# Kernel optimization log

Hardware: AMD Instinct MI355X
Metric: run time of the kernel (lower is better)

The kernel has to match this reference:

```python
import jax, jax.numpy as jnp
import numpy as np

D_MODEL = 768
N_HEADS = 24
D_HEAD = 64
D_STATE = 64
CHUNK = 64
D_INNER = N_HEADS * D_HEAD  # 1536
N_LAYER = 24
B_SZ = 2
SEQ = 8192
RMS_EPS = 1.1920929e-07  # torch.finfo(float32).eps (nn.RMSNorm default eps)


def setup_inputs() -> dict:
    key = jax.random.key(0)
    ks = jax.random.split(key, 8)
    proj = N_HEADS * (1 + 2 * D_STATE)
    return {
        "hidden_states": jax.random.normal(ks[0], (B_SZ, SEQ, D_MODEL), jnp.float32),
        "norm_w": jnp.ones((D_MODEL,), jnp.float32),
        "in_proj_w": jax.random.normal(ks[1], (2 * D_INNER, D_MODEL), jnp.float32) * 0.02,
        "in_proj_b": jnp.zeros((2 * D_INNER,), jnp.float32),
        "conv_w": jax.random.normal(ks[2], (D_INNER, 1, 4), jnp.float32) * 0.25,
        "conv_b": jnp.zeros((D_INNER,), jnp.float32),
        "x_proj_w": jax.random.normal(ks[3], (proj, D_INNER), jnp.float32) * 0.02,
        "x_proj_b": jnp.zeros((proj,), jnp.float32),
        "A_log": jnp.full((N_HEADS,), float(np.log(0.5)), jnp.float32),
        "log2_alpha_base": jnp.full((N_HEADS,), -0.15, jnp.float32),
        "log2_beta": jnp.zeros((N_HEADS,), jnp.float32),
        "surprise_ema": jnp.ones((N_HEADS,), jnp.float32),
        "out_proj_w": jax.random.normal(ks[4], (D_MODEL, D_INNER), jnp.float32) * 0.02,
        "out_proj_b": jnp.zeros((D_MODEL,), jnp.float32),
        "res_gate": jnp.full((1,), 1.0 / float(np.sqrt(2 * N_LAYER)), jnp.float32),
    }


def _block_forward(hidden_states, norm_w, in_proj_w, in_proj_b, conv_w, conv_b,
                   x_proj_w, x_proj_b, A_log, log2_alpha_base, log2_beta,
                   surprise_ema, out_proj_w, out_proj_b, res_gate):
    residual = hidden_states
    b, L, _ = hidden_states.shape

    # RMSNorm
    x = hidden_states * jax.lax.rsqrt(
        jnp.mean(hidden_states ** 2, axis=-1, keepdims=True) + RMS_EPS) * norm_w

    # in_proj, split x/z
    xz = hidden_states_proj = x @ in_proj_w.T + in_proj_b
    x, z = jnp.split(xz, 2, axis=-1)  # [b, L, d_inner] each

    # causal depthwise conv1d (kernel 4, padding 3, then truncate to L)
    xc = jnp.transpose(x, (0, 2, 1))  # [b, C, L]
    xc = jax.lax.conv_general_dilated(
        xc, conv_w, window_strides=(1,), padding=[(3, 3)],
        dimension_numbers=("NCH", "OIH", "NCH"), feature_group_count=D_INNER)
    xc = xc[:, :, :L] + conv_b[None, :, None]
    x = jax.nn.silu(jnp.transpose(xc, (0, 2, 1)))  # [b, L, d_inner]

    # x_proj -> dt, B, C
    xp = (x @ x_proj_w.T + x_proj_b).reshape(b, L, N_HEADS, 1 + 2 * D_STATE)
    dt = xp[..., 0]
    B_ssm = xp[..., 1:1 + D_STATE]
    C_ssm = xp[..., 1 + D_STATE:]
    B_ssm = B_ssm / jnp.maximum(jnp.linalg.norm(B_ssm, axis=-1, keepdims=True), 1e-12)
    C_ssm = C_ssm / jnp.maximum(jnp.linalg.norm(C_ssm, axis=-1, keepdims=True), 1e-12)

    A = jnp.clip(A_log, -2.3, -0.01)[None, None, :]  # [1,1,H]
    dt_scale = jnp.clip(jax.nn.softplus(jnp.clip(dt, -10.0, 10.0)), 0.01, 10.0)
    A = jnp.clip(A * dt_scale, -20.0, -0.001)  # [b, L, H]

    X = x.reshape(b, L, N_HEADS, D_HEAD)

    # ---- chunked surprise-gated SSD (L divisible by CHUNK) ----
    n = L // CHUNK
    X_t = X.reshape(b, n, CHUNK, N_HEADS, D_HEAD).transpose(0, 3, 1, 2, 4)      # b h n c d
    A_t = A.reshape(b, n, CHUNK, N_HEADS).transpose(0, 3, 1, 2)                 # b h n c
    B_t = B_ssm.reshape(b, n, CHUNK, N_HEADS, D_STATE).transpose(0, 3, 1, 2, 4) # b h n c s
    C_t = C_ssm.reshape(b, n, CHUNK, N_HEADS, D_STATE).transpose(0, 3, 1, 2, 4) # b h n c s

    BX = jnp.einsum("bhncs,bhncd->bhnsd", B_t, X_t)
    chunk_surprise = jnp.mean(BX ** 2, axis=(-1, -2))  # [b, h, n]

    # surprise gate (training=True: EMA updated first, no_grad)
    mean_s = jax.lax.stop_gradient(jnp.mean(chunk_surprise, axis=(0, 2)))
    ema = 0.99 * surprise_ema + 0.01 * mean_s
    normalized = chunk_surprise / (ema[None, :, None] + 1e-6)
    alpha_base = 1.0 - 2.0 ** jnp.clip(log2_alpha_base, -3.32, -0.015)  # [H]
    beta = 2.0 ** jnp.clip(log2_beta, -2.0, 2.0)                        # [H]
    boost_pos = jax.nn.relu(jnp.tanh(beta[None, :, None] * normalized))
    ab = alpha_base[None, :, None]
    alpha = jnp.clip(ab + (1.0 - ab) * boost_pos, 0.01, 0.999)          # [b, h, n]

    A_mod = A_t * (1.0 - alpha)[..., None]          # b h n c
    A_cs = jnp.cumsum(A_mod, axis=-1)               # b h n c

    # intra-chunk: L[i,j] = exp(cs_i - cs_j) for i >= j
    diff = A_cs[..., :, None] - A_cs[..., None, :]  # b h n c c
    mask = jnp.tril(jnp.ones((CHUNK, CHUNK), bool))
    Lmat = jnp.where(mask, jnp.exp(diff), 0.0)
    CB = jnp.einsum("bhnid,bhnjd->bhnij", C_t, B_t)
    Y_intra = jnp.einsum("bhnij,bhnjd->bhnid", Lmat * CB, X_t)

    # inter-chunk recurrence
    decay_chunk = jnp.exp(jnp.sum(A_mod, axis=-1))              # b h n
    decay_to_end = jnp.exp(A_cs[..., -1:] - A_cs)               # b h n c
    h_chunk_final = jnp.einsum("bhnc,bhncs,bhncd->bhnsd",
                               decay_to_end, B_t, X_t)           # b h n s d

    def step(carry, inp):
        d, hf = inp  # d: [b,h], hf: [b,h,s,d]
        new = d[..., None, None] * carry + hf
        return new, carry  # emit state BEFORE this chunk

    carry0 = jnp.zeros((b, N_HEADS, D_STATE, D_HEAD), X.dtype)
    _, h_inter = jax.lax.scan(
        step, carry0,
        (decay_chunk.transpose(2, 0, 1), h_chunk_final.transpose(2, 0, 1, 3, 4)))
    h_inter = h_inter.transpose(1, 2, 0, 3, 4)  # b h n s d

    decay_from_start = jnp.exp(A_cs)  # b h n c
    Y_inter = jnp.einsum("bhnis,bhnsp,bhni->bhnip", C_t, h_inter, decay_from_start)

    Y = (Y_intra + Y_inter).transpose(0, 2, 3, 1, 4).reshape(b, L, D_INNER)

    # gate + out proj + gated residual
    y = jnp.clip(Y, -100.0, 100.0) * jax.nn.sigmoid(z)
    out = jnp.clip(y @ out_proj_w.T + out_proj_b, -100.0, 100.0)
    return residual + out * res_gate


def reference(hidden_states, norm_w, in_proj_w, in_proj_b, conv_w, conv_b,
              x_proj_w, x_proj_b, A_log, log2_alpha_base, log2_beta,
              surprise_ema, out_proj_w, out_proj_b, res_gate):
    return _block_forward(hidden_states, norm_w, in_proj_w, in_proj_b, conv_w,
                          conv_b, x_proj_w, x_proj_b, A_log, log2_alpha_base,
                          log2_beta, surprise_ema, out_proj_w, out_proj_b, res_gate)
```

## Files before the change

### kernel.cpp

```cpp
#include <hip/hip_runtime.h>
#include <hip/hip_bf16.h>
#include <cstdint>
#include <cstddef>

#define L_SEQ   8192
#define DMODEL  768
#define NHEADS  24
#define DINNER  1536
#define NPROJ   3096
#define NPROJP  3200
#define NPROJ2  3264
#define HSTR    136
#define NTOK    16384
#define SEG_T   4096
#define NSEG    4
#define RMS_EPS 1.1920929e-07f

typedef __hip_bfloat16 bf16;
typedef __attribute__((ext_vector_type(8))) short bf8v;
typedef __attribute__((ext_vector_type(4))) float f4v;

__device__ __forceinline__ float clampf(float x, float lo, float hi) {
    return fminf(fmaxf(x, lo), hi);
}
__device__ __forceinline__ float bf2f(bf16 v) { return __bfloat162float(v); }
__device__ __forceinline__ bf16  f2bf(float v) { return __float2bfloat16(v); }
__device__ __forceinline__ short f2bs(float v) {
    bf16 b = __float2bfloat16(v);
    return *reinterpret_cast<short*>(&b);
}
__device__ __forceinline__ float bs2f(short v) {
    return __uint_as_float(((unsigned)(unsigned short)v) << 16);
}
__device__ __forceinline__ void st1(float* p, float v) { *p = v; }
__device__ __forceinline__ void st1(bf16* p, float v) { *p = f2bf(v); }
__device__ __forceinline__ void st4(bf16* p, float4 v) {
    p[0] = f2bf(v.x); p[1] = f2bf(v.y); p[2] = f2bf(v.z); p[3] = f2bf(v.w);
}

#define GLOAD16(gsrc, ldst) __builtin_amdgcn_global_load_lds( \
    (const __attribute__((address_space(1))) void*)(gsrc),    \
    (__attribute__((address_space(3))) void*)(ldst), 16, 0, 0)

__global__ __launch_bounds__(256) void k_cvt(const float* __restrict__ s,
                                             bf16* __restrict__ d, int n4) {
    int i = blockIdx.x * 256 + threadIdx.x;
    if (i < n4) {
        float4 v = *(const float4*)&s[i * 4];
        st4(&d[i * 4], v);
    }
}
__global__ __launch_bounds__(256) void k_zero(bf16* __restrict__ d, int n) {
    int i = blockIdx.x * 256 + threadIdx.x;
    if (i < n) d[i] = f2bf(0.f);
}

__global__ __launch_bounds__(256) void k_rmsnorm(const float* __restrict__ hs,
                                                 const float* __restrict__ w,
                                                 bf16* __restrict__ xn) {
    int t = blockIdx.x;
    const float* p = hs + (size_t)t * DMODEL;
    float s = 0.f;
    for (int i = threadIdx.x; i < DMODEL; i += 256) { float v = p[i]; s += v * v; }
    for (int off = 32; off; off >>= 1) s += __shfl_xor(s, off, 64);
    __shared__ float ws4[4];
    int lane = threadIdx.x & 63, wv = threadIdx.x >> 6;
    if (lane == 0) ws4[wv] = s;
    __syncthreads();
    s = ws4[0] + ws4[1] + ws4[2] + ws4[3];
    float r = 1.0f / sqrtf(s * (1.0f / DMODEL) + RMS_EPS);
    bf16* o = xn + (size_t)t * DMODEL;
    for (int i = threadIdx.x; i < DMODEL; i += 256) o[i] = f2bf(p[i] * r * w[i]);
}

template <typename TC, int EPI>
__global__ __launch_bounds__(256) void k_mgemm(const bf16* __restrict__ A,
                                               const bf16* __restrict__ B,
                                               const float* __restrict__ bias,
                                               TC* __restrict__ C,
                                               int M, int N, int K,
                                               const float* __restrict__ resid,
                                               const float* __restrict__ gatep) {
    __shared__ short As[2][128 * 32];
    __shared__ short Bs[2][128 * 32];
    int tid = threadIdx.x;
    int lane = tid & 63, w = tid >> 6;

    int gx = gridDim.x, gy = gridDim.y;
    int bid = blockIdx.y * gx + blockIdx.x;
    int xcd = bid & 7, idx = bid >> 3;
    int bys = gy >> 3;
    int gby = bys < 8 ? bys : 8;
    int sg  = idx / (gx * gby);
    int rem = idx - sg * (gx * gby);
    int bx  = rem / gby;
    int byl = rem - bx * gby;
    int by  = xcd * bys + sg * gby + byl;
    int m0 = by * 128, n0 = bx * 128;

    int wm = (w >> 1) << 6, wn = (w & 1) << 6;

    const size_t rowskip = (size_t)16 * K * 2;
    const char* Ag = (const char*)(A + (size_t)(m0 + (w << 5) + (lane >> 2)) * K) + (lane & 3) * 16;
    const char* Bg = (const char*)(B + (size_t)(n0 + (w << 5) + (lane >> 2)) * K) + (lane & 3) * 16;
    short* Al0 = &As[0][(w << 5) * 32];
    short* Bl0 = &Bs[0][(w << 5) * 32];
    short* Al1 = &As[1][(w << 5) * 32];
    short* Bl1 = &Bs[1][(w << 5) * 32];

    f4v acc[4][4];
#pragma unroll
    for (int i = 0; i < 4; ++i)
#pragma unroll
        for (int j = 0; j < 4; ++j) acc[i][j] = (f4v){0.f, 0.f, 0.f, 0.f};

    auto stage = [&](int buf, int k0) {
        size_t kb = (size_t)k0 * 2;
        short* Al = buf ? Al1 : Al0;
        short* Bl = buf ? Bl1 : Bl0;
        GLOAD16(Ag + kb,           Al);
        GLOAD16(Ag + kb + rowskip, Al + 16 * 32);
        GLOAD16(Bg + kb,           Bl);
        GLOAD16(Bg + kb + rowskip, Bl + 16 * 32);
    };

    stage(0, 0);
    int cur = 0;
    int row16 = lane & 15, kg = (lane >> 4) << 3;
    for (int k0 = 0; k0 < K; k0 += 32) {
        __syncthreads();
        if (k0 + 32 < K) stage(cur ^ 1, k0 + 32);
        const short* Ab = As[cur];
        const short* Bb = Bs[cur];
        bf8v af[4], bfv[4];
#pragma unroll
        for (int fm = 0; fm < 4; ++fm)
            af[fm] = *(const bf8v*)&Ab[(wm + (fm << 4) + row16) * 32 + kg];
#pragma unroll
        for (int fn = 0; fn < 4; ++fn)
            bfv[fn] = *(const bf8v*)&Bb[(wn + (fn << 4) + row16) * 32 + kg];
#pragma unroll
        for (int fm = 0; fm < 4; ++fm)
#pragma unroll
            for (int fn = 0; fn < 4; ++fn)
                acc[fm][fn] = __builtin_amdgcn_mfma_f32_16x16x32_bf16(
                    af[fm], bfv[fn], acc[fm][fn], 0, 0, 0);
        cur ^= 1;
    }

    float gate = (EPI == 1) ? *gatep : 0.f;
    int rbase = m0 + wm + ((lane >> 4) << 2);
#pragma unroll
    for (int fn = 0; fn < 4; ++fn) {
        int col = n0 + wn + (fn << 4) + (lane & 15);
        if (col >= N) continue;
        float bc = bias[col];
        int dst = col;
        if (EPI == 2) {
            int hh = col / 129, q = col - hh * 129;
            dst = hh * HSTR + (q == 0 ? 0 : q + 7);
        }
#pragma unroll
        for (int fm = 0; fm < 4; ++fm) {
#pragma unroll
            for (int r = 0; r < 4; ++r) {
                int row = rbase + (fm << 4) + r;
                float v = acc[fm][fn][r] + bc;
                if (EPI == 1) {
                    v = resid[(size_t)row * N + col] + clampf(v, -100.f, 100.f) * gate;
                    st1(&C[(size_t)row * N + col], v);
                } else if (EPI == 2) {
                    st1(&C[(size_t)row * NPROJ2 + dst], v);
                } else {
                    st1(&C[(size_t)row * N + col], v);
                }
            }
        }
    }
}

__global__ __launch_bounds__(256) void k_save_halo(const bf16* __restrict__ x,
                                                   bf16* __restrict__ dst) {
    int i = blockIdx.x * 256 + threadIdx.x;
    if (i < 3 * DINNER) dst[i] = x[(size_t)(SEG_T - 3) * DINNER + i];
}

__global__ __launch_bounds__(192) void k_conv8(const bf16* __restrict__ x,
                                               const float* __restrict__ cw,
                                               const float* __restrict__ cb,
                                               bf16* __restrict__ xc) {
    int c0 = threadIdx.x * 8;
    int r  = blockIdx.x;
    int l  = r & (L_SEQ - 1);
    float acc[8];
#pragma unroll
    for (int j = 0; j < 8; ++j) acc[j] = cb[c0 + j];
#pragma unroll
    for (int k = 0; k < 4; ++k) {
        int lp = l - 3 + k;
        if (lp < 0) continue;
        bf8v v = *(const bf8v*)(const void*)(x + (size_t)(r - 3 + k) * DINNER + c0);
#pragma unroll
        for (int j = 0; j < 8; ++j)
            acc[j] += cw[(c0 + j) * 4 + k] * bs2f(v[j]);
    }
    bf8v o;
#pragma unroll
    for (int j = 0; j < 8; ++j) {
        float a = acc[j];
        o[j] = f2bs(a / (1.f + expf(-a)));
    }
    *(bf8v*)(xc + (size_t)r * DINNER + c0) = o;
}

__global__ __launch_bounds__(256) void k_conv_silu(const bf16* __restrict__ x,
                                                   const bf16* __restrict__ xh,
                                                   const float* __restrict__ cw,
                                                   const float* __restrict__ cb,
                                                   bf16* __restrict__ xc,
                                                   int l0) {
    int c = blockIdx.x * 256 + threadIdx.x;
    int r = blockIdx.y;
    int l = l0 + r;
    float acc = cb[c];
#pragma unroll
    for (int k = 0; k < 4; ++k) {
        int lp = l - 3 + k;
        if (lp < 0) continue;
        float v = (lp < l0) ? bf2f(xh[(size_t)(lp - l0 + 3) * DINNER + c])
                            : bf2f(x[(size_t)(lp - l0) * DINNER + c]);
        acc += cw[c * 4 + k] * v;
    }
    float sig = 1.f / (1.f + expf(-acc));
    xc[(size_t)r * DINNER + c] = f2bf(acc * sig);
}

__global__ __launch_bounds__(256) void k_prep(const bf16* __restrict__ xp,
                                              const float* __restrict__ A_log,
                                              float* __restrict__ Aarr,
                                              float* __restrict__ invB,
                                              float* __restrict__ invC) {
    int wv = threadIdx.x >> 6, lane = threadIdx.x & 63;
    int idx = blockIdx.x * 4 + wv;
    int t = idx / 24, h = idx - t * 24;
    const bf16* base = xp + (size_t)t * NPROJ2 + h * HSTR;
    float b = bf2f(base[8 + lane]), c = bf2f(base[72 + lane]);
    float sb = b * b, sc = c * c;
    for (int off = 32; off; off >>= 1) {
        sb += __shfl_xor(sb, off, 64);
        sc += __shfl_xor(sc, off, 64);
    }
    if (lane == 0) {
        invB[idx] = 1.f / fmaxf(sqrtf(sb), 1e-12f);
        invC[idx] = 1.f / fmaxf(sqrtf(sc), 1e-12f);
        float dt = clampf(bf2f(base[0]), -10.f, 10.f);
        float dts = clampf(log1pf(expf(dt)), 0.01f, 10.f);
        float A = clampf(A_log[h], -2.3f, -0.01f) * dts;
        Aarr[idx] = clampf(A, -20.f, -0.001f);
    }
}

__global__ __launch_bounds__(256) void k_surprise_all(const bf16* __restrict__ xp,
                                                      const bf16* __restrict__ xc,
                                                      const float* __restrict__ invB,
                                                      float* __restrict__ cs) {
    int g = blockIdx.x;
    int cg = g / 24, h = g - cg * 24;
    int b = cg >> 7, nl = cg & 127;
    int t0 = cg * 64;
    size_t cs_idx = (size_t)(b * 24 + h) * 128 + nl;
    __shared__ short Ws[64 * 72];
    __shared__ short Xt[64 * 72];
    int tid = threadIdx.x;
#pragma unroll
    for (int half = 0; half < 2; ++half) {
        int tau = tid + half * 256;
        int c = tau >> 3, s0 = (tau & 7) << 3;
        int t = t0 + c;
        float ib = invB[t * 24 + h];
        bf8v Bv = *(const bf8v*)(const void*)(xp + (size_t)t * NPROJ2 + h * HSTR + 8 + s0);
        bf8v Xv = *(const bf8v*)(const void*)(xc + (size_t)t * DINNER + h * 64 + s0);
#pragma unroll
        for (int u = 0; u < 8; ++u) {
            Ws[(s0 + u) * 72 + c] = f2bs(bs2f(Bv[u]) * ib);
            Xt[(s0 + u) * 72 + c] = Xv[u];
        }
    }
    __syncthreads();
    int w = tid >> 6, lane = tid & 63;
    int r16 = lane & 15, kq = (lane >> 4) << 3;
    int strip = w << 4;
    f4v acc[4];
#pragma unroll
    for (int dt = 0; dt < 4; ++dt) acc[dt] = (f4v){0.f, 0.f, 0.f, 0.f};
#pragma unroll
    for (int ks = 0; ks < 2; ++ks) {
        bf8v af = *(const bf8v*)&Ws[(strip + r16) * 72 + ks * 32 + kq];
#pragma unroll
        for (int dt = 0; dt < 4; ++dt) {
            bf8v bf_ = *(const bf8v*)&Xt[((dt << 4) + r16) * 72 + ks * 32 + kq];
            acc[dt] = __builtin_amdgcn_mfma_f32_16x16x32_bf16(af, bf_, acc[dt], 0, 0, 0);
        }
    }
    float ss = 0.f;
#pragma unroll
    for (int dt = 0; dt < 4; ++dt)
#pragma unroll
        for (int r = 0; r < 4; ++r) ss += acc[dt][r] * acc[dt][r];
    for (int off = 32; off; off >>= 1) ss += __shfl_xor(ss, off, 64);
    __shared__ float ws4[4];
    if (lane == 0) ws4[w] = ss;
    __syncthreads();
    if (tid == 0) cs[cs_idx] = (ws4[0] + ws4[1] + ws4[2] + ws4[3]) * (1.f / 4096.f);
}

__global__ __launch_bounds__(256) void k_alpha(const float* __restrict__ cs,
                                               const float* __restrict__ ema0,
                                               const float* __restrict__ l2ab,
                                               const float* __restrict__ l2b,
                                               float* __restrict__ alpha) {
    int h = blockIdx.x, tid = threadIdx.x;
    int b = tid >> 7, n = tid & 127;
    int gi = (b * 24 + h) * 128 + n;
    float v = cs[gi];
    float s = v;
    for (int off = 32; off; off >>= 1) s += __shfl_xor(s, off, 64);
    __shared__ float ws4[4];
    int lane = tid & 63, wv = tid >> 6;
    if (lane == 0) ws4[wv] = s;
    __syncthreads();
    float total = ws4[0] + ws4[1] + ws4[2] + ws4[3];
    float ema = 0.99f * ema0[h] + 0.01f * (total * (1.f / 256.f));
    float ab = 1.f - exp2f(clampf(l2ab[h], -3.32f, -0.015f));
    float beta = exp2f(clampf(l2b[h], -2.f, 2.f));
    float nz = v / (ema + 1e-6f);
    float boost = fmaxf(tanhf(beta * nz), 0.f);
    alpha[gi] = clampf(ab + (1.f - ab) * boost, 0.01f, 0.999f);
}

__device__ __forceinline__ void chunk_body(const bf16* xp, const bf16* xc,
                                           const float* invB, const float* invC,
                                           const float* Aarr, const float* alpha,
                                           bf16* ybuf, bf16* hf, float* dchunk,
                                           int t0, int h, size_t gidx, size_t hbase) {
    float alp = alpha[gidx];
    __shared__ short Cs[64 * 72];
    __shared__ short Bs[64 * 72];
    __shared__ short Ws[64 * 72];
    __shared__ short Xt[64 * 72];
    __shared__ float Acs[64];
    __shared__ float dte[64];
    int tid = threadIdx.x;
    if (tid < 64) {
        float a = Aarr[(size_t)(t0 + tid) * 24 + h] * (1.f - alp);
        for (int off = 1; off < 64; off <<= 1) {
            float u = __shfl_up(a, off, 64);
            if (tid >= off) a += u;
        }
        Acs[tid] = a;
        float total = __shfl(a, 63, 64);
        dte[tid] = expf(total - a);
        if (tid == 0) dchunk[gidx] = expf(total);
    }
    __syncthreads();
#pragma unroll
    for (int half = 0; half < 2; ++half) {
        int tau = tid + half * 256;
        int c = tau >> 3, s0 = (tau & 7) << 3;
        int t = t0 + c;
        const bf16* bp = xp + (size_t)t * NPROJ2 + h * HSTR;
        float ib = invB[t * 24 + h], ic2 = invC[t * 24 + h];
        float dc = dte[c];
        bf8v Bv = *(const bf8v*)(const void*)(bp + 8 + s0);
        bf8v Cv = *(const bf8v*)(const void*)(bp + 72 + s0);
        bf8v Xv = *(const bf8v*)(const void*)(xc + (size_t)t * DINNER + h * 64 + s0);
        bf8v Bsc, Csc;
#pragma unroll
        for (int u = 0; u < 8; ++u) {
            float bv = bs2f(Bv[u]) * ib;
            Bsc[u] = f2bs(bv);
            Csc[u] = f2bs(bs2f(Cv[u]) * ic2);
            Ws[(s0 + u) * 72 + c] = f2bs(bv * dc);
            Xt[(s0 + u) * 72 + c] = Xv[u];
        }
        *(bf8v*)&Bs[c * 72 + s0] = Bsc;
        *(bf8v*)&Cs[c * 72 + s0] = Csc;
    }
    __syncthreads();
    int w = tid >> 6, lane = tid & 63;
    int r16 = lane & 15, kq = (lane >> 4) << 3;
    int strip = w << 4;
    f4v acb[4], ach[4];
#pragma unroll
    for (int jt = 0; jt < 4; ++jt) {
        acb[jt] = (f4v){0.f, 0.f, 0.f, 0.f};
        ach[jt] = (f4v){0.f, 0.f, 0.f, 0.f};
    }
#pragma unroll
    for (int ks = 0; ks < 2; ++ks) {
        bf8v afc = *(const bf8v*)&Cs[(strip + r16) * 72 + ks * 32 + kq];
        bf8v afw = *(const bf8v*)&Ws[(strip + r16) * 72 + ks * 32 + kq];
#pragma unroll
        for (int jt = 0; jt < 4; ++jt) {
            bf8v bb = *(const bf8v*)&Bs[((jt << 4) + r16) * 72 + ks * 32 + kq];
            acb[jt] = __builtin_amdgcn_mfma_f32_16x16x32_bf16(afc, bb, acb[jt], 0, 0, 0);
            bf8v xx = *(const bf8v*)&Xt[((jt << 4) + r16) * 72 + ks * 32 + kq];
            ach[jt] = __builtin_amdgcn_mfma_f32_16x16x32_bf16(afw, xx, ach[jt], 0, 0, 0);
        }
    }
    int rbase = strip + ((lane >> 4) << 2);
#pragma unroll
    for (int dt = 0; dt < 4; ++dt) {
        int d = (dt << 4) + r16;
#pragma unroll
        for (int r = 0; r < 4; ++r)
            hf[hbase + (size_t)(rbase + r) * 64 + d] = f2bf(ach[dt][r]);
    }
    __syncthreads();
    short* Ms = Cs;
#pragma unroll
    for (int jt = 0; jt < 4; ++jt) {
        int j = (jt << 4) + r16;
        float aj = Acs[j];
#pragma unroll
        for (int r = 0; r < 4; ++r) {
            int i = rbase + r;
            float m = (j <= i) ? expf(Acs[i] - aj) * acb[jt][r] : 0.f;
            Ms[i * 72 + j] = f2bs(m);
        }
    }
    __syncthreads();
    f4v acy[4];
#pragma unroll
    for (int dt = 0; dt < 4; ++dt) acy[dt] = (f4v){0.f, 0.f, 0.f, 0.f};
#pragma unroll
    for (int ks = 0; ks < 2; ++ks) {
        bf8v afm = *(const bf8v*)&Ms[(strip + r16) * 72 + ks * 32 + kq];
#pragma unroll
        for (int dt = 0; dt < 4; ++dt) {
            bf8v xx = *(const bf8v*)&Xt[((dt << 4) + r16) * 72 + ks * 32 + kq];
            acy[dt] = __builtin_amdgcn_mfma_f32_16x16x32_bf16(afm, xx, acy[dt], 0, 0, 0);
        }
    }
#pragma unroll
    for (int dt = 0; dt < 4; ++dt) {
        int d = (dt << 4) + r16;
#pragma unroll
        for (int r = 0; r < 4; ++r) {
            int i = rbase + r;
            ybuf[(size_t)(t0 + i) * DINNER + h * 64 + d] = f2bf(acy[dt][r]);
        }
    }
}

__global__ __launch_bounds__(256) void k_chunk(const bf16* __restrict__ xp,
                                               const bf16* __restrict__ xc,
                                               const float* __restrict__ invB,
                                               const float* __restrict__ invC,
                                               const float* __restrict__ Aarr,
                                               const float* __restrict__ alpha,
                                               bf16* __restrict__ ybuf,
                                               bf16* __restrict__ hf,
                                               float* __restrict__ dchunk,
                                               int b, int l0) {
    int g = blockIdx.x;
    int h = g >> 6, nl = g & 63;
    chunk_body(xp, xc, invB, invC, Aarr, alpha, ybuf, hf, dchunk,
               nl * 64, h,
               (size_t)(b * 24 + h) * 128 + (l0 >> 6) + nl,
               (size_t)((h << 6) + nl) * 4096);
}

__global__ __launch_bounds__(256) void k_chunk_all(const bf16* __restrict__ xp,
                                                   const bf16* __restrict__ xc,
                                                   const float* __restrict__ invB,
                                                   const float* __restrict__ invC,
                                                   const float* __restrict__ Aarr,
                                                   const float* __restrict__ alpha,
                                                   bf16* __restrict__ ybuf,
                                                   bf16* __restrict__ hf,
                                                   float* __restrict__ dchunk) {
    int g = blockIdx.x;
    int bh = g >> 7, nl = g & 127;
    int b = bh >= 24 ? 1 : 0, h = bh - b * 24;
    size_t gidx = (size_t)bh * 128 + nl;
    chunk_body(xp, xc, invB, invC, Aarr, alpha, ybuf, hf, dchunk,
               b * L_SEQ + nl * 64, h, gidx, gidx * 4096);
}

__global__ __launch_bounds__(256) void k_scan(bf16* __restrict__ hf,
                                              const float* __restrict__ dchunk,
                                              float* __restrict__ carry,
                                              int b, int l0, int nch) {
    int h = blockIdx.x >> 4;
    int e = ((blockIdx.x & 15) << 8) + threadIdx.x;
    int bh = b * 24 + h;
    float c = (l0 == 0) ? 0.f : carry[(size_t)bh * 4096 + e];
    size_t a = (size_t)h * nch * 4096 + e;
    float v = bf2f(hf[a]);
    const float* dcp = dchunk + (size_t)bh * 128 + (l0 >> 6);
    for (int nl = 0; nl < nch; ++nl) {
        float dc = dcp[nl];
        float vn = (nl + 1 < nch) ? bf2f(hf[a + 4096]) : 0.f;
        hf[a] = f2bf(c);
        c = dc * c + v;
        v = vn;
        a += 4096;
    }
    carry[(size_t)bh * 4096 + e] = c;
}

__global__ __launch_bounds__(256) void k_scan_all(bf16* __restrict__ hf,
                                                  const float* __restrict__ dchunk) {
    int bh = blockIdx.x >> 4;
    int e = ((blockIdx.x & 15) << 8) + threadIdx.x;
    float c = 0.f;
    size_t a = (size_t)bh * 128 * 4096 + e;
    float v = bf2f(hf[a]);
    const float* dcp = dchunk + (size_t)bh * 128;
    for (int nl = 0; nl < 128; ++nl) {
        float dc = dcp[nl];
        float vn = (nl + 1 < 128) ? bf2f(hf[a + 4096]) : 0.f;
        hf[a] = f2bf(c);
        c = dc * c + v;
        v = vn;
        a += 4096;
    }
}

__device__ __forceinline__ void inter_body(const bf16* xp, const float* invC,
                                           const float* Aarr, const float* alpha,
                                           const bf16* hf, const bf16* zbuf,
                                           bf16* ybuf,
                                           int t0, int h, size_t gidx, size_t hbase) {
    float alp = alpha[gidx];
    __shared__ short Cs[64 * 72];
    __shared__ short Ht[64 * 72];
    __shared__ float dfs[64];
    int tid = threadIdx.x;
    if (tid < 64) {
        float a = Aarr[(size_t)(t0 + tid) * 24 + h] * (1.f - alp);
        for (int off = 1; off < 64; off <<= 1) {
            float u = __shfl_up(a, off, 64);
            if (tid >= off) a += u;
        }
        dfs[tid] = expf(a);
    }
#pragma unroll
    for (int half = 0; half < 2; ++half) {
        int tau = tid + half * 256;
        int c = tau >> 3, s0 = (tau & 7) << 3;
        int t = t0 + c;
        float ic2 = invC[t * 24 + h];
        bf8v Cv = *(const bf8v*)(const void*)(xp + (size_t)t * NPROJ2 + h * HSTR + 72 + s0);
        bf8v Hv = *(const bf8v*)(const void*)(hf + hbase + (size_t)c * 64 + s0);
        bf8v Csc;
#pragma unroll
        for (int u = 0; u < 8; ++u) {
            Csc[u] = f2bs(bs2f(Cv[u]) * ic2);
            Ht[(s0 + u) * 72 + c] = Hv[u];
        }
        *(bf8v*)&Cs[c * 72 + s0] = Csc;
    }
    __syncthreads();
    int w = tid >> 6, lane = tid & 63;
    int r16 = lane & 15, kq = (lane >> 4) << 3;
    int strip = w << 4;
    f4v acc[4];
#pragma unroll
    for (int dt = 0; dt < 4; ++dt) acc[dt] = (f4v){0.f, 0.f, 0.f, 0.f};
#pragma unroll
    for (int ks = 0; ks < 2; ++ks) {
        bf8v af = *(const bf8v*)&Cs[(strip + r16) * 72 + ks * 32 + kq];
#pragma unroll
        for (int dt = 0; dt < 4; ++dt) {
            bf8v hfr = *(const bf8v*)&Ht[((dt << 4) + r16) * 72 + ks * 32 + kq];
            acc[dt] = __builtin_amdgcn_mfma_f32_16x16x32_bf16(af, hfr, acc[dt], 0, 0, 0);
        }
    }
    int ibase = strip + ((lane >> 4) << 2);
#pragma unroll
    for (int dt = 0; dt < 4; ++dt) {
        int d = (dt << 4) + r16;
#pragma unroll
        for (int r = 0; r < 4; ++r) {
            int i = ibase + r;
            float df = dfs[i];
            size_t yoff = (size_t)(t0 + i) * DINNER + h * 64 + d;
            float Y = clampf(bf2f(ybuf[yoff]) + df * acc[dt][r], -100.f, 100.f);
            float zz = bf2f(zbuf[yoff]);
            ybuf[yoff] = f2bf(Y / (1.f + expf(-zz)));
        }
    }
}

__global__ __launch_bounds__(256) void k_inter(const bf16* __restrict__ xp,
                                               const float* __restrict__ invC,
                                               const float* __restrict__ Aarr,
                                               const float* __restrict__ alpha,
                                               const bf16* __restrict__ hf,
                                               const bf16* __restrict__ zbuf,
                                               bf16* __restrict__ ybuf,
                                               int b, int l0) {
    int g = blockIdx.x;
    int h = g >> 6, nl = g & 63;
    inter_body(xp, invC, Aarr, alpha, hf, zbuf, ybuf,
               nl * 64, h,
               (size_t)(b * 24 + h) * 128 + (l0 >> 6) + nl,
               (size_t)((h << 6) + nl) * 4096);
}

__global__ __launch_bounds__(256) void k_inter_all(const bf16* __restrict__ xp,
                                                   const float* __restrict__ invC,
                                                   const float* __restrict__ Aarr,
                                                   const float* __restrict__ alpha,
                                                   const bf16* __restrict__ hf,
                                                   const bf16* __restrict__ zbuf,
                                                   bf16* __restrict__ ybuf) {
    int g = blockIdx.x;
    int bh = g >> 7, nl = g & 127;
    int b = bh >= 24 ? 1 : 0, h = bh - b * 24;
    size_t gidx = (size_t)bh * 128 + nl;
    inter_body(xp, invC, Aarr, alpha, hf, zbuf, ybuf,
               b * L_SEQ + nl * 64, h, gidx, gidx * 4096);
}

extern "C" void kernel_launch(void* const* d_in, const int* in_sizes, int n_in,
                              void* d_out, int out_size, void* d_ws, size_t ws_size,
                              hipStream_t stream) {
    const float* hs     = (const float*)d_in[0];
    const float* norm_w = (const float*)d_in[1];
    const float* w1     = (const float*)d_in[2];
    const float* b1     = (const float*)d_in[3];
    const float* cw     = (const float*)d_in[4];
    const float* cbias  = (const float*)d_in[5];
    const float* w2     = (const float*)d_in[6];
    const float* b2     = (const float*)d_in[7];
    const float* A_log  = (const float*)d_in[8];
    const float* l2ab   = (const float*)d_in[9];
    const float* l2b    = (const float*)d_in[10];
    const float* ema0   = (const float*)d_in[11];
    const float* w3     = (const float*)d_in[12];
    const float* b3     = (const float*)d_in[13];
    const float* rg     = (const float*)d_in[14];
    float* out = (float*)d_out;

    const bool FULL = ws_size >= (size_t)255500000;
    const size_t YROWS = FULL ? (size_t)NTOK : (size_t)SEG_T;

    char* base = (char*)d_ws;
    size_t off = 0;
    auto alloc = [&](size_t bytes) -> void* {
        void* p = base + off;
        off += (bytes + 255) & ~(size_t)255;
        return p;
    };
    bf16* w1bf  = (bf16*)alloc((size_t)2 * DINNER * DMODEL * 2);
    bf16* w2bf  = (bf16*)alloc((size_t)NPROJP * DINNER * 2);
    bf16* w3bf  = (bf16*)alloc((size_t)DMODEL * DINNER * 2);
    bf16* xn    = (bf16*)alloc((size_t)NTOK * DMODEL * 2);
    bf16* ybuf  = (bf16*)alloc(YROWS * DINNER * 2);
    bf16* hf    = (bf16*)alloc(YROWS / 64 * NHEADS * 4096 * 2);
    bf16* xhalo = (bf16*)alloc((size_t)2 * 3 * DINNER * 2);
    float* cs   = (float*)alloc((size_t)6144 * 4);
    float* alp  = (float*)alloc((size_t)6144 * 4);
    float* dch  = (float*)alloc((size_t)6144 * 4);
    float* carry= (float*)alloc((size_t)48 * 4096 * 4);
    bf16* xp    = (bf16*)alloc((size_t)NTOK * NPROJ2 * 2);
    float* Aarr = (float*)alloc((size_t)NTOK * 24 * 4);
    float* invB = (float*)alloc((size_t)NTOK * 24 * 4);
    float* invC = (float*)alloc((size_t)NTOK * 24 * 4);
    bf16* xbuf  = ybuf;
    bf16* xc_all = (bf16*)d_out;

    {
        int n1 = 2 * DINNER * DMODEL / 4, n2 = NPROJ * DINNER / 4, n3 = DMODEL * DINNER / 4;
        k_cvt<<<(n1 + 255) / 256, 256, 0, stream>>>(w1, w1bf, n1);
        k_cvt<<<(n2 + 255) / 256, 256, 0, stream>>>(w2, w2bf, n2);
        k_cvt<<<(n3 + 255) / 256, 256, 0, stream>>>(w3, w3bf, n3);
        int nz = (NPROJP - NPROJ) * DINNER;
        k_zero<<<(nz + 255) / 256, 256, 0, stream>>>(w2bf + (size_t)NPROJ * DINNER, nz);
    }

    const dim3 gPall(NPROJP / 128, NTOK / 128);

    if (FULL) {
        const dim3 gX16(DINNER / 128, NTOK / 128);
        const dim3 gO16(DMODEL / 128, NTOK / 128);
        k_rmsnorm<<<NTOK, 256, 0, stream>>>(hs, norm_w, xn);
        k_mgemm<bf16, 0><<<gX16, 256, 0, stream>>>(xn, w1bf, b1, xbuf,
                                                   NTOK, DINNER, DMODEL, nullptr, nullptr);
        k_conv8<<<NTOK, 192, 0, stream>>>(xbuf, cw, cbias, xc_all);
        k_mgemm<bf16, 2><<<gPall, 256, 0, stream>>>(xc_all, w2bf, b2, xp,
                                                    NTOK, NPROJ, DINNER, nullptr, nullptr);
        k_prep<<<NTOK * 24 / 4, 256, 0, stream>>>(xp, A_log, Aarr, invB, invC);
        k_surprise_all<<<6144, 256, 0, stream>>>(xp, xc_all, invB, cs);
        k_alpha<<<24, 256, 0, stream>>>(cs, ema0, l2ab, l2b, alp);

        k_chunk_all<<<6144, 256, 0, stream>>>(xp, xc_all, invB, invC, Aarr, alp,
                                              ybuf, hf, dch);
        k_mgemm<bf16, 0><<<gX16, 256, 0, stream>>>(xn, w1bf + (size_t)DINNER * DMODEL,
                                                   b1 + DINNER, xc_all,
                                                   NTOK, DINNER, DMODEL, nullptr, nullptr);
        k_scan_all<<<768, 256, 0, stream>>>(hf, dch);
        k_inter_all<<<6144, 256, 0, stream>>>(xp, invC, Aarr, alp, hf, xc_all, ybuf);
        k_mgemm<float, 1><<<gO16, 256, 0, stream>>>(ybuf, w3bf, b3, out,
                                                    NTOK, DMODEL, DINNER, hs, rg);
        return;
    }

    const dim3 gX(DINNER / 128, SEG_T / 128);
    const dim3 gO(DMODEL / 128, SEG_T / 128);

    k_rmsnorm<<<NTOK, 256, 0, stream>>>(hs, norm_w, xn);
    for (int s = 0; s < NSEG; ++s) {
        size_t t0 = (size_t)s * SEG_T;
        int l0 = (int)(t0 & (L_SEQ - 1));
        bf16* xc = xc_all + t0 * DINNER;
        k_mgemm<bf16, 0><<<gX, 256, 0, stream>>>(xn + t0 * DMODEL, w1bf, b1, xbuf,
                                                 SEG_T, DINNER, DMODEL, nullptr, nullptr);
        k_save_halo<<<18, 256, 0, stream>>>(xbuf, xhalo + (size_t)((s + 1) & 1) * 3 * DINNER);
        k_conv_silu<<<dim3(DINNER / 256, SEG_T), 256, 0, stream>>>(
            xbuf, xhalo + (size_t)(s & 1) * 3 * DINNER, cw, cbias, xc, l0);
    }
    k_mgemm<bf16, 2><<<gPall, 256, 0, stream>>>(xc_all, w2bf, b2, xp,
                                                NTOK, NPROJ, DINNER, nullptr, nullptr);
    k_prep<<<NTOK * 24 / 4, 256, 0, stream>>>(xp, A_log, Aarr, invB, invC);
    k_surprise_all<<<6144, 256, 0, stream>>>(xp, xc_all, invB, cs);
    k_alpha<<<24, 256, 0, stream>>>(cs, ema0, l2ab, l2b, alp);

    for (int s = 0; s < NSEG; ++s) {
        size_t t0 = (size_t)s * SEG_T;
        int l0 = (int)(t0 & (L_SEQ - 1));
        int b  = (int)(t0 >> 13);
        const float* hseg = hs + t0 * DMODEL;
        bf16* xc = xc_all + t0 * DINNER;
        bf16* zseg = xc;
        const bf16* xpS = xp + t0 * NPROJ2;
        const float* AarrS = Aarr + t0 * 24;
        const float* invBS = invB + t0 * 24;
        const float* invCS = invC + t0 * 24;
        k_chunk<<<NHEADS * 64, 256, 0, stream>>>(xpS, xc, invBS, invCS, AarrS, alp,
                                                 ybuf, hf, dch, b, l0);
        k_mgemm<bf16, 0><<<gX, 256, 0, stream>>>(xn + t0 * DMODEL,
                                                 w1bf + (size_t)DINNER * DMODEL,
                                                 b1 + DINNER, zseg,
                                                 SEG_T, DINNER, DMODEL, nullptr, nullptr);
        k_scan<<<384, 256, 0, stream>>>(hf, dch, carry, b, l0, 64);
        k_inter<<<NHEADS * 64, 256, 0, stream>>>(xpS, invCS, AarrS, alp, hf, zseg,
                                                 ybuf, b, l0);
        k_mgemm<float, 1><<<gO, 256, 0, stream>>>(ybuf, w3bf, b3, out + t0 * DMODEL,
                                                  SEG_T, DMODEL, DINNER, hseg, rg);
    }
}
```

Measured before the change: 907.4 us.

## Segment by batch, compact projection buffer, and split dt into its own array

This removes the dual FULL/segmented schedule and always processes the two batch sequences one after another, in 8192-token segments. Each segment aligns with a sequence boundary, so the halo-save kernel and the scalar conv kernel go away in favour of the vectorised conv8 kernel. The x_proj output is packed to a 3072-wide B/C layout, and dt is written by the GEMM epilogue into a separate small buffer, which cuts padding and read traffic. In exchange, RMSNorm is recomputed per segment to keep the normalised buffer small. The schedule also uses more launches than a single full-size pass.

Measured after the change: 932.0 us. 2.7% more time.

```diff
diff --git a/kernel.cpp b/kernel.cpp
--- a/kernel.cpp
+++ b/kernel.cpp
@@ -9,11 +9,9 @@
 #define DINNER  1536
 #define NPROJ   3096
 #define NPROJP  3200
-#define NPROJ2  3264
-#define HSTR    136
+#define XPS     3072
 #define NTOK    16384
-#define SEG_T   4096
-#define NSEG    4
+#define BT      8192
 #define RMS_EPS 1.1920929e-07f
 
 typedef __hip_bfloat16 bf16;
@@ -80,7 +78,8 @@
                                                TC* __restrict__ C,
                                                int M, int N, int K,
                                                const float* __restrict__ resid,
-                                               const float* __restrict__ gatep) {
+                                               const float* __restrict__ gatep,
+                                               bf16* __restrict__ dtb) {
     __shared__ short As[2][128 * 32];
     __shared__ short Bs[2][128 * 32];
     int tid = threadIdx.x;
@@ -155,10 +154,11 @@
         int col = n0 + wn + (fn << 4) + (lane & 15);
         if (col >= N) continue;
         float bc = bias[col];
-        int dst = col;
+        int hh = 0, dst = col;
         if (EPI == 2) {
-            int hh = col / 129, q = col - hh * 129;
-            dst = hh * HSTR + (q == 0 ? 0 : q + 7);
+            hh = col / 129;
+            int q = col - hh * 129;
+            dst = (q == 0) ? -1 : hh * 128 + q - 1;
         }
 #pragma unroll
         for (int fm = 0; fm < 4; ++fm) {
@@ -170,19 +170,14 @@
                     v = resid[(size_t)row * N + col] + clampf(v, -100.f, 100.f) * gate;
                     st1(&C[(size_t)row * N + col], v);
                 } else if (EPI == 2) {
-                    st1(&C[(size_t)row * NPROJ2 + dst], v);
+                    if (dst < 0) dtb[(size_t)row * 24 + hh] = f2bf(v);
+                    else st1(&C[(size_t)row * XPS + dst], v);
                 } else {
                     st1(&C[(size_t)row * N + col], v);
                 }
             }
         }
     }
-}
-
-__global__ __launch_bounds__(256) void k_save_halo(const bf16* __restrict__ x,
-                                                   bf16* __restrict__ dst) {
-    int i = blockIdx.x * 256 + threadIdx.x;
-    if (i < 3 * DINNER) dst[i] = x[(size_t)(SEG_T - 3) * DINNER + i];
 }
 
 __global__ __launch_bounds__(192) void k_conv8(const bf16* __restrict__ x,
@@ -191,15 +186,14 @@
                                                bf16* __restrict__ xc) {
     int c0 = threadIdx.x * 8;
     int r  = blockIdx.x;
-    int l  = r & (L_SEQ - 1);
     float acc[8];
 #pragma unroll
     for (int j = 0; j < 8; ++j) acc[j] = cb[c0 + j];
 #pragma unroll
     for (int k = 0; k < 4; ++k) {
-        int lp = l - 3 + k;
+        int lp = r - 3 + k;
         if (lp < 0) continue;
-        bf8v v = *(const bf8v*)(const void*)(x + (size_t)(r - 3 + k) * DINNER + c0);
+        bf8v v = *(const bf8v*)(const void*)(x + (size_t)lp * DINNER + c0);
 #pragma unroll
         for (int j = 0; j < 8; ++j)
             acc[j] += cw[(c0 + j) * 4 + k] * bs2f(v[j]);
@@ -213,29 +207,8 @@
     *(bf8v*)(xc + (size_t)r * DINNER + c0) = o;
 }
 
-__global__ __launch_bounds__(256) void k_conv_silu(const bf16* __restrict__ x,
-                                                   const bf16* __restrict__ xh,
-                                                   const float* __restrict__ cw,
-                                                   const float* __restrict__ cb,
-                                                   bf16* __restrict__ xc,
-                                                   int l0) {
-    int c = blockIdx.x * 256 + threadIdx.x;
-    int r = blockIdx.y;
-    int l = l0 + r;
-    float acc = cb[c];
-#pragma unroll
-    for (int k = 0; k < 4; ++k) {
-        int lp = l - 3 + k;
-        if (lp < 0) continue;
-        float v = (lp < l0) ? bf2f(xh[(size_t)(lp - l0 + 3) * DINNER + c])
-                            : bf2f(x[(size_t)(lp - l0) * DINNER + c]);
-        acc += cw[c * 4 + k] * v;
-    }
-    float sig = 1.f / (1.f + expf(-acc));
-    xc[(size_t)r * DINNER + c] = f2bf(acc * sig);
-}
-
 __global__ __launch_bounds__(256) void k_prep(const bf16* __restrict__ xp,
+                                              const bf16* __restrict__ dtb,
                                               const float* __restrict__ A_log,
                                               float* __restrict__ Aarr,
                                               float* __restrict__ invB,
@@ -243,8 +216,8 @@
     int wv = threadIdx.x >> 6, lane = threadIdx.x & 63;
     int idx = blockIdx.x * 4 + wv;
     int t = idx / 24, h = idx - t * 24;
-    const bf16* base = xp + (size_t)t * NPROJ2 + h * HSTR;
-    float b = bf2f(base[8 + lane]), c = bf2f(base[72 + lane]);
+    const bf16* base = xp + (size_t)t * XPS + h * 128;
+    float b = bf2f(base[lane]), c = bf2f(base[64 + lane]);
     float sb = b * b, sc = c * c;
     for (int off = 32; off; off >>= 1) {
         sb += __shfl_xor(sb, off, 64);
@@ -253,7 +226,7 @@
     if (lane == 0) {
         invB[idx] = 1.f / fmaxf(sqrtf(sb), 1e-12f);
         invC[idx] = 1.f / fmaxf(sqrtf(sc), 1e-12f);
-        float dt = clampf(bf2f(base[0]), -10.f, 10.f);
+        float dt = clampf(bf2f(dtb[idx]), -10.f, 10.f);
         float dts = clampf(log1pf(expf(dt)), 0.01f, 10.f);
         float A = clampf(A_log[h], -2.3f, -0.01f) * dts;
         Aarr[idx] = clampf(A, -20.f, -0.001f);
@@ -278,7 +251,7 @@
         int c = tau >> 3, s0 = (tau & 7) << 3;
         int t = t0 + c;
         float ib = invB[t * 24 + h];
-        bf8v Bv = *(const bf8v*)(const void*)(xp + (size_t)t * NPROJ2 + h * HSTR + 8 + s0);
+        bf8v Bv = *(const bf8v*)(const void*)(xp + (size_t)t * XPS + h * 128 + s0);
         bf8v Xv = *(const bf8v*)(const void*)(xc + (size_t)t * DINNER + h * 64 + s0);
 #pragma unroll
         for (int u = 0; u < 8; ++u) {
@@ -338,11 +311,21 @@
     alpha[gi] = clampf(ab + (1.f - ab) * boost, 0.01f, 0.999f);
 }
 
-__device__ __forceinline__ void chunk_body(const bf16* xp, const bf16* xc,
-                                           const float* invB, const float* invC,
-                                           const float* Aarr, const float* alpha,
-                                           bf16* ybuf, bf16* hf, float* dchunk,
-                                           int t0, int h, size_t gidx, size_t hbase) {
+__global__ __launch_bounds__(256) void k_chunk(const bf16* __restrict__ xp,
+                                               const bf16* __restrict__ xc,
+                                               const float* __restrict__ invB,
+                                               const float* __restrict__ invC,
+                                               const float* __restrict__ Aarr,
+                                               const float* __restrict__ alpha,
+                                               bf16* __restrict__ ybuf,
+                                               bf16* __restrict__ hf,
+                                               float* __restrict__ dchunk,
+                                               int b) {
+    int g = blockIdx.x;
+    int h = g >> 7, nl = g & 127;
+    int t0 = nl * 64;
+    size_t gidx = (size_t)(b * 24 + h) * 128 + nl;
+    size_t hbase = (size_t)g * 4096;
     float alp = alpha[gidx];
     __shared__ short Cs[64 * 72];
     __shared__ short Bs[64 * 72];
@@ -368,11 +351,11 @@
         int tau = tid + half * 256;
         int c = tau >> 3, s0 = (tau & 7) << 3;
         int t = t0 + c;
-        const bf16* bp = xp + (size_t)t * NPROJ2 + h * HSTR;
+        const bf16* bp = xp + (size_t)t * XPS + h * 128;
         float ib = invB[t * 24 + h], ic2 = invC[t * 24 + h];
         float dc = dte[c];
-        bf8v Bv = *(const bf8v*)(const void*)(bp + 8 + s0);
-        bf8v Cv = *(const bf8v*)(const void*)(bp + 72 + s0);
+        bf8v Bv = *(const bf8v*)(const void*)(bp + s0);
+        bf8v Cv = *(const bf8v*)(const void*)(bp + 64 + s0);
         bf8v Xv = *(const bf8v*)(const void*)(xc + (size_t)t * DINNER + h * 64 + s0);
         bf8v Bsc, Csc;
 #pragma unroll
@@ -453,71 +436,15 @@
     }
 }
 
-__global__ __launch_bounds__(256) void k_chunk(const bf16* __restrict__ xp,
-                                               const bf16* __restrict__ xc,
-                                               const float* __restrict__ invB,
-                                               const float* __restrict__ invC,
-                                               const float* __restrict__ Aarr,
-                                               const float* __restrict__ alpha,
-                                               bf16* __restrict__ ybuf,
-                                               bf16* __restrict__ hf,
-                                               float* __restrict__ dchunk,
-                                               int b, int l0) {
-    int g = blockIdx.x;
-    int h = g >> 6, nl = g & 63;
-    chunk_body(xp, xc, invB, invC, Aarr, alpha, ybuf, hf, dchunk,
-               nl * 64, h,
-               (size_t)(b * 24 + h) * 128 + (l0 >> 6) + nl,
-               (size_t)((h << 6) + nl) * 4096);
-}
-
-__global__ __launch_bounds__(256) void k_chunk_all(const bf16* __restrict__ xp,
-                                                   const bf16* __restrict__ xc,
-                                                   const float* __restrict__ invB,
-                                                   const float* __restrict__ invC,
-                                                   const float* __restrict__ Aarr,
-                                                   const float* __restrict__ alpha,
-                                                   bf16* __restrict__ ybuf,
-                                                   bf16* __restrict__ hf,
-                                                   float* __restrict__ dchunk) {
-    int g = blockIdx.x;
-    int bh = g >> 7, nl = g & 127;
-    int b = bh >= 24 ? 1 : 0, h = bh - b * 24;
-    size_t gidx = (size_t)bh * 128 + nl;
-    chunk_body(xp, xc, invB, invC, Aarr, alpha, ybuf, hf, dchunk,
-               b * L_SEQ + nl * 64, h, gidx, gidx * 4096);
-}
-
 __global__ __launch_bounds__(256) void k_scan(bf16* __restrict__ hf,
                                               const float* __restrict__ dchunk,
-                                              float* __restrict__ carry,
-                                              int b, int l0, int nch) {
+                                              int b) {
     int h = blockIdx.x >> 4;
     int e = ((blockIdx.x & 15) << 8) + threadIdx.x;
-    int bh = b * 24 + h;
-    float c = (l0 == 0) ? 0.f : carry[(size_t)bh * 4096 + e];
-    size_t a = (size_t)h * nch * 4096 + e;
+    float c = 0.f;
+    size_t a = (size_t)h * 128 * 4096 + e;
     float v = bf2f(hf[a]);
-    const float* dcp = dchunk + (size_t)bh * 128 + (l0 >> 6);
-    for (int nl = 0; nl < nch; ++nl) {
-        float dc = dcp[nl];
-        float vn = (nl + 1 < nch) ? bf2f(hf[a + 4096]) : 0.f;
-        hf[a] = f2bf(c);
-        c = dc * c + v;
-        v = vn;
-        a += 4096;
-    }
-    carry[(size_t)bh * 4096 + e] = c;
-}
-
-__global__ __launch_bounds__(256) void k_scan_all(bf16* __restrict__ hf,
-                                                  const float* __restrict__ dchunk) {
-    int bh = blockIdx.x >> 4;
-    int e = ((blockIdx.x & 15) << 8) + threadIdx.x;
-    float c = 0.f;
-    size_t a = (size_t)bh * 128 * 4096 + e;
-    float v = bf2f(hf[a]);
-    const float* dcp = dchunk + (size_t)bh * 128;
+    const float* dcp = dchunk + (size_t)(b * 24 + h) * 128;
     for (int nl = 0; nl < 128; ++nl) {
         float dc = dcp[nl];
         float vn = (nl + 1 < 128) ? bf2f(hf[a + 4096]) : 0.f;
@@ -528,11 +455,19 @@
     }
 }
 
-__device__ __forceinline__ void inter_body(const bf16* xp, const float* invC,
-                                           const float* Aarr, const float* alpha,
-                                           const bf16* hf, const bf16* zbuf,
-                                           bf16* ybuf,
-                                           int t0, int h, size_t gidx, size_t hbase) {
+__global__ __launch_bounds__(256) void k_inter(const bf16* __restrict__ xp,
+                                               const float* __restrict__ invC,
+                                               const float* __restrict__ Aarr,
+                                               const float* __restrict__ alpha,
+                                               const bf16* __restrict__ hf,
+                                               const bf16* __restrict__ zbuf,
+                                               bf16* __restrict__ ybuf,
+                                               int b) {
+    int g = blockIdx.x;
+    int h = g >> 7, nl = g & 127;
+    int t0 = nl * 64;
+    size_t gidx = (size_t)(b * 24 + h) * 128 + nl;
+    size_t hbase = (size_t)g * 4096;
     float alp = alpha[gidx];
     __shared__ short Cs[64 * 72];
     __shared__ short Ht[64 * 72];
@@ -552,7 +487,7 @@
         int c = tau >> 3, s0 = (tau & 7) << 3;
         int t = t0 + c;
         float ic2 = invC[t * 24 + h];
-        bf8v Cv = *(const bf8v*)(const void*)(xp + (size_t)t * NPROJ2 + h * HSTR + 72 + s0);
+        bf8v Cv = *(const bf8v*)(const void*)(xp + (size_t)t * XPS + h * 128 + 64 + s0);
         bf8v Hv = *(const bf8v*)(const void*)(hf + hbase + (size_t)c * 64 + s0);
         bf8v Csc;
 #pragma unroll
@@ -592,37 +527,6 @@
             ybuf[yoff] = f2bf(Y / (1.f + expf(-zz)));
         }
     }
-}
-
-__global__ __launch_bounds__(256) void k_inter(const bf16* __restrict__ xp,
-                                               const float* __restrict__ invC,
-                                               const float* __restrict__ Aarr,
-                                               const float* __restrict__ alpha,
-                                               const bf16* __restrict__ hf,
-                                               const bf16* __restrict__ zbuf,
-                                               bf16* __restrict__ ybuf,
-                                               int b, int l0) {
-    int g = blockIdx.x;
-    int h = g >> 6, nl = g & 63;
-    inter_body(xp, invC, Aarr, alpha, hf, zbuf, ybuf,
-               nl * 64, h,
-               (size_t)(b * 24 + h) * 128 + (l0 >> 6) + nl,
-               (size_t)((h << 6) + nl) * 4096);
-}
-
-__global__ __launch_bounds__(256) void k_inter_all(const bf16* __restrict__ xp,
-                                                   const float* __restrict__ invC,
-                                                   const float* __restrict__ Aarr,
-                                                   const float* __restrict__ alpha,
-                                                   const bf16* __restrict__ hf,
-                                                   const bf16* __restrict__ zbuf,
-                                                   bf16* __restrict__ ybuf) {
-    int g = blockIdx.x;
-    int bh = g >> 7, nl = g & 127;
-    int b = bh >= 24 ? 1 : 0, h = bh - b * 24;
-    size_t gidx = (size_t)bh * 128 + nl;
-    inter_body(xp, invC, Aarr, alpha, hf, zbuf, ybuf,
-               b * L_SEQ + nl * 64, h, gidx, gidx * 4096);
 }
 
 extern "C" void kernel_launch(void* const* d_in, const int* in_sizes, int n_in,
@@ -645,9 +549,6 @@
     const float* rg     = (const float*)d_in[14];
     float* out = (float*)d_out;
 
-    const bool FULL = ws_size >= (size_t)255500000;
-    const size_t YROWS = FULL ? (size_t)NTOK : (size_t)SEG_T;
-
     char* base = (char*)d_ws;
     size_t off = 0;
     auto alloc = [&](size_t bytes) -> void* {
@@ -658,15 +559,14 @@
     bf16* w1bf  = (bf16*)alloc((size_t)2 * DINNER * DMODEL * 2);
     bf16* w2bf  = (bf16*)alloc((size_t)NPROJP * DINNER * 2);
     bf16* w3bf  = (bf16*)alloc((size_t)DMODEL * DINNER * 2);
-    bf16* xn    = (bf16*)alloc((size_t)NTOK * DMODEL * 2);
-    bf16* ybuf  = (bf16*)alloc(YROWS * DINNER * 2);
-    bf16* hf    = (bf16*)alloc(YROWS / 64 * NHEADS * 4096 * 2);
-    bf16* xhalo = (bf16*)alloc((size_t)2 * 3 * DINNER * 2);
+    bf16* xnb   = (bf16*)alloc((size_t)BT * DMODEL * 2);
+    bf16* ybuf  = (bf16*)alloc((size_t)BT * DINNER * 2);
+    bf16* hf    = (bf16*)alloc((size_t)NHEADS * 128 * 4096 * 2);
+    bf16* dtb   = (bf16*)alloc((size_t)NTOK * 24 * 2);
     float* cs   = (float*)alloc((size_t)6144 * 4);
     float* alp  = (float*)alloc((size_t)6144 * 4);
     float* dch  = (float*)alloc((size_t)6144 * 4);
-    float* carry= (float*)alloc((size_t)48 * 4096 * 4);
-    bf16* xp    = (bf16*)alloc((size_t)NTOK * NPROJ2 * 2);
+    bf16* xp    = (bf16*)alloc((size_t)NTOK * XPS * 2);
     float* Aarr = (float*)alloc((size_t)NTOK * 24 * 4);
     float* invB = (float*)alloc((size_t)NTOK * 24 * 4);
     float* invC = (float*)alloc((size_t)NTOK * 24 * 4);
@@ -682,74 +582,41 @@
         k_zero<<<(nz + 255) / 256, 256, 0, stream>>>(w2bf + (size_t)NPROJ * DINNER, nz);
     }
 
+    const dim3 gXb(DINNER / 128, BT / 128);
+    const dim3 gOb(DMODEL / 128, BT / 128);
     const dim3 gPall(NPROJP / 128, NTOK / 128);
 
-    if (FULL) {
-        const dim3 gX16(DINNER / 128, NTOK / 128);
-        const dim3 gO16(DMODEL / 128, NTOK / 128);
-        k_rmsnorm<<<NTOK, 256, 0, stream>>>(hs, norm_w, xn);
-        k_mgemm<bf16, 0><<<gX16, 256, 0, stream>>>(xn, w1bf, b1, xbuf,
-                                                   NTOK, DINNER, DMODEL, nullptr, nullptr);
-        k_conv8<<<NTOK, 192, 0, stream>>>(xbuf, cw, cbias, xc_all);
-        k_mgemm<bf16, 2><<<gPall, 256, 0, stream>>>(xc_all, w2bf, b2, xp,
-                                                    NTOK, NPROJ, DINNER, nullptr, nullptr);
-        k_prep<<<NTOK * 24 / 4, 256, 0, stream>>>(xp, A_log, Aarr, invB, invC);
-        k_surprise_all<<<6144, 256, 0, stream>>>(xp, xc_all, invB, cs);
-        k_alpha<<<24, 256, 0, stream>>>(cs, ema0, l2ab, l2b, alp);
-
-        k_chunk_all<<<6144, 256, 0, stream>>>(xp, xc_all, invB, invC, Aarr, alp,
-                                              ybuf, hf, dch);
-        k_mgemm<bf16, 0><<<gX16, 256, 0, stream>>>(xn, w1bf + (size_t)DINNER * DMODEL,
-                                                   b1 + DINNER, xc_all,
-                                                   NTOK, DINNER, DMODEL, nullptr, nullptr);
-        k_scan_all<<<768, 256, 0, stream>>>(hf, dch);
-        k_inter_all<<<6144, 256, 0, stream>>>(xp, invC, Aarr, alp, hf, xc_all, ybuf);
-        k_mgemm<float, 1><<<gO16, 256, 0, stream>>>(ybuf, w3bf, b3, out,
-                                                    NTOK, DMODEL, DINNER, hs, rg);
-        return;
-    }
-
-    const dim3 gX(DINNER / 128, SEG_T / 128);
-    const dim3 gO(DMODEL / 128, SEG_T / 128);
-
-    k_rmsnorm<<<NTOK, 256, 0, stream>>>(hs, norm_w, xn);
-    for (int s = 0; s < NSEG; ++s) {
-        size_t t0 = (size_t)s * SEG_T;
-        int l0 = (int)(t0 & (L_SEQ - 1));
-        bf16* xc = xc_all + t0 * DINNER;
-        k_mgemm<bf16, 0><<<gX, 256, 0, stream>>>(xn + t0 * DMODEL, w1bf, b1, xbuf,
-                                                 SEG_T, DINNER, DMODEL, nullptr, nullptr);
-        k_save_halo<<<18, 256, 0, stream>>>(xbuf, xhalo + (size_t)((s + 1) & 1) * 3 * DINNER);
-        k_conv_silu<<<dim3(DINNER / 256, SEG_T), 256, 0, stream>>>(
-            xbuf, xhalo + (size_t)(s & 1) * 3 * DINNER, cw, cbias, xc, l0);
+    for (int bt = 0; bt < 2; ++bt) {
+        size_t t0 = (size_t)bt * BT;
+        k_rmsnorm<<<BT, 256, 0, stream>>>(hs + t0 * DMODEL, norm_w, xnb);
+        k_mgemm<bf16, 0><<<gXb, 256, 0, stream>>>(xnb, w1bf, b1, xbuf,
+                                                  BT, DINNER, DMODEL, nullptr, nullptr, nullptr);
+        k_conv8<<<BT, 192, 0, stream>>>(xbuf, cw, cbias, xc_all + t0 * DINNER);
     }
     k_mgemm<bf16, 2><<<gPall, 256, 0, stream>>>(xc_all, w2bf, b2, xp,
-                                                NTOK, NPROJ, DINNER, nullptr, nullptr);
-    k_prep<<<NTOK * 24 / 4, 256, 0, stream>>>(xp, A_log, Aarr, invB, invC);
+                                                NTOK, NPROJ, DINNER, nullptr, nullptr, dtb);
+    k_prep<<<NTOK * 24 / 4, 256, 0, stream>>>(xp, dtb, A_log, Aarr, invB, invC);
     k_surprise_all<<<6144, 256, 0, stream>>>(xp, xc_all, invB, cs);
     k_alpha<<<24, 256, 0, stream>>>(cs, ema0, l2ab, l2b, alp);
 
-    for (int s = 0; s < NSEG; ++s) {
-        size_t t0 = (size_t)s * SEG_T;
-        int l0 = (int)(t0 & (L_SEQ - 1));
-        int b  = (int)(t0 >> 13);
-        const float* hseg = hs + t0 * DMODEL;
+    for (int bt = 0; bt < 2; ++bt) {
+        size_t t0 = (size_t)bt * BT;
         bf16* xc = xc_all + t0 * DINNER;
         bf16* zseg = xc;
-        const bf16* xpS = xp + t0 * NPROJ2;
+        const bf16* xpS = xp + t0 * XPS;
         const float* AarrS = Aarr + t0 * 24;
         const float* invBS = invB + t0 * 24;
         const float* invCS = invC + t0 * 24;
-        k_chunk<<<NHEADS * 64, 256, 0, stream>>>(xpS, xc, invBS, invCS, AarrS, alp,
-                                                 ybuf, hf, dch, b, l0);
-        k_mgemm<bf16, 0><<<gX, 256, 0, stream>>>(xn + t0 * DMODEL,
-                                                 w1bf + (size_t)DINNER * DMODEL,
-                                                 b1 + DINNER, zseg,
-                                                 SEG_T, DINNER, DMODEL, nullptr, nullptr);
-        k_scan<<<384, 256, 0, stream>>>(hf, dch, carry, b, l0, 64);
-        k_inter<<<NHEADS * 64, 256, 0, stream>>>(xpS, invCS, AarrS, alp, hf, zseg,
-                                                 ybuf, b, l0);
-        k_mgemm<float, 1><<<gO, 256, 0, stream>>>(ybuf, w3bf, b3, out + t0 * DMODEL,
-                                                  SEG_T, DMODEL, DINNER, hseg, rg);
-    }
-}
+        k_chunk<<<NHEADS * 128, 256, 0, stream>>>(xpS, xc, invBS, invCS, AarrS, alp,
+                                                  ybuf, hf, dch, bt);
+        k_rmsnorm<<<BT, 256, 0, stream>>>(hs + t0 * DMODEL, norm_w, xnb);
+        k_mgemm<bf16, 0><<<gXb, 256, 0, stream>>>(xnb, w1bf + (size_t)DINNER * DMODEL,
+                                                  b1 + DINNER, zseg,
+                                                  BT, DINNER, DMODEL, nullptr, nullptr, nullptr);
+        k_scan<<<384, 256, 0, stream>>>(hf, dch, bt);
+        k_inter<<<NHEADS * 128, 256, 0, stream>>>(xpS, invCS, AarrS, alp, hf, zseg, ybuf, bt);
+        k_mgemm<float, 1><<<gOb, 256, 0, stream>>>(ybuf, w3bf, b3, out + t0 * DMODEL,
+                                                   BT, DMODEL, DINNER,
+                                                   hs + t0 * DMODEL, rg, nullptr);
+    }
+}
```
